# Kernel tuning notes

Hardware: AMD Instinct MI355X
Metric: run time of the kernel (lower is better)

Reference implementation:

```python
import jax, jax.numpy as jnp
import numpy as np

D = 1024
H = 16
DK = D // H
TB = 64  # temporal_bias_dim
SCALE = DK ** -0.5


def setup_inputs() -> dict:
    key = jax.random.key(0)
    ks = jax.random.split(key, 12)
    B, S = 8, 512
    s = 0.02
    return {
        "x": jax.random.normal(ks[0], (B, S, D), jnp.float32),
        "padding_masks": jnp.ones((B, 1, 1, S), jnp.int32),
        "batch_temporal_mat": jax.random.uniform(ks[1], (B, S, S), jnp.float32) * 100.0,
        "wq": jax.random.normal(ks[2], (D, D), jnp.float32) * s,
        "bq": jnp.zeros((D,), jnp.float32),
        "wk": jax.random.normal(ks[3], (D, D), jnp.float32) * s,
        "bk": jnp.zeros((D,), jnp.float32),
        "wv": jax.random.normal(ks[4], (D, D), jnp.float32) * s,
        "bv": jnp.zeros((D,), jnp.float32),
        "w_proj": jax.random.normal(ks[5], (D, D), jnp.float32) * s,
        "b_proj": jnp.zeros((D,), jnp.float32),
        "w_tb1": jax.random.normal(ks[6], (1, TB), jnp.float32) * 0.5,
        "b_tb1": jnp.zeros((TB,), jnp.float32),
        "w_tb2": jax.random.normal(ks[7], (TB, 1), jnp.float32) * 0.5,
        "b_tb2": jnp.zeros((1,), jnp.float32),
    }


def reference(x, padding_masks, batch_temporal_mat, wq, bq, wk, bk, wv, bv,
              w_proj, b_proj, w_tb1, b_tb1, w_tb2, b_tb2):
    B, S, _ = x.shape

    def heads(w, b):
        return (x @ w + b).reshape(B, S, H, DK).transpose(0, 2, 1, 3)  # (B,H,S,DK)

    q, k, v = heads(wq, bq), heads(wk, bk), heads(wv, bv)
    scores = jnp.einsum("bhqd,bhkd->bhqk", q, k) * SCALE  # (B,H,S,S)

    # temporal bias: 1/log(e + t) -> Linear(1,64) -> leaky_relu(0.2) -> Linear(64,1)
    t = 1.0 / jnp.log(jnp.exp(jnp.float32(1.0)) + batch_temporal_mat)  # (B,S,S)
    h = t[..., None] * w_tb1[0] + b_tb1  # (B,S,S,TB)
    h = jnp.where(h >= 0, h, 0.2 * h)
    bias = (h @ w_tb2)[..., 0] + b_tb2[0]  # (B,S,S)
    scores = scores + bias[:, None, :, :]

    neg_inf = jnp.float32(-jnp.inf)
    scores = jnp.where(padding_masks == 0, neg_inf, scores)
    causal = jnp.triu(jnp.ones((S, S), bool), k=1)  # (S,S), add_cls=False
    scores = jnp.where(causal[None, None], neg_inf, scores)

    p_attn = jax.nn.softmax(scores, axis=-1)
    out = jnp.einsum("bhqk,bhkd->bhqd", p_attn, v)
    out = out.transpose(0, 2, 1, 3).reshape(B, S, D)
    out = out @ w_proj + b_proj
    return out
```

## Files before the change

kernel.cpp:

```cpp
#include <hip/hip_runtime.h>
#include <hip/hip_bf16.h>

#define B_  8
#define S_  512
#define D_  1024
#define H_  16
#define DK_ 64
#define TB_ 64
#define SCALE_ 0.125f

typedef __attribute__((ext_vector_type(8))) short          bh8;
typedef __attribute__((ext_vector_type(4))) float          f32x4;
typedef __attribute__((ext_vector_type(8))) unsigned short us8;

__device__ __forceinline__ unsigned short f2bf(float f) {
    unsigned u = __float_as_uint(f);
    unsigned r = 0x7fffu + ((u >> 16) & 1u);
    return (unsigned short)((u + r) >> 16);
}

__device__ __forceinline__ void gl16(const unsigned short* g, unsigned short* l) {
    __builtin_amdgcn_global_load_lds(
        (const __attribute__((address_space(1))) void*)g,
        (__attribute__((address_space(3))) void*)l, 16, 0, 0);
}

__global__ __launch_bounds__(256)
void cvt_x_kernel(const float* __restrict__ in, unsigned short* __restrict__ out, int n8)
{
    int i = blockIdx.x * 256 + threadIdx.x;
    if (i >= n8) return;
    float4 a = *(const float4*)&in[(size_t)i * 8];
    float4 b = *(const float4*)&in[(size_t)i * 8 + 4];
    us8 o;
    o[0] = f2bf(a.x); o[1] = f2bf(a.y); o[2] = f2bf(a.z); o[3] = f2bf(a.w);
    o[4] = f2bf(b.x); o[5] = f2bf(b.y); o[6] = f2bf(b.z); o[7] = f2bf(b.w);
    *(us8*)&out[(size_t)i * 8] = o;
}

__global__ __launch_bounds__(256)
void cvt_wt4_kernel(const float* __restrict__ w0, const float* __restrict__ w1,
                    const float* __restrict__ w2, const float* __restrict__ w3,
                    unsigned short* __restrict__ o0, unsigned short* __restrict__ o1,
                    unsigned short* __restrict__ o2, unsigned short* __restrict__ o3)
{
    __shared__ float t[64][65];
    const int z = blockIdx.z;
    const float* W = (z == 0) ? w0 : (z == 1) ? w1 : (z == 2) ? w2 : w3;
    unsigned short* Wt = (z == 0) ? o0 : (z == 1) ? o1 : (z == 2) ? o2 : o3;
    const int bx = blockIdx.x, by = blockIdx.y;
    const int c  = threadIdx.x & 63;
    const int r0 = threadIdx.x >> 6;
    #pragma unroll
    for (int i = 0; i < 16; ++i) {
        int r = r0 + i * 4;
        t[r][c] = W[(size_t)(by * 64 + r) * 1024 + bx * 64 + c];
    }
    __syncthreads();
    #pragma unroll
    for (int i = 0; i < 16; ++i) {
        int r = r0 + i * 4;
        Wt[(size_t)(bx * 64 + r) * 1024 + by * 64 + c] = f2bf(t[c][r]);
    }
}

__global__ __launch_bounds__(256)
void gemm_qkv_kernel(const unsigned short* __restrict__ A,
                     const unsigned short* __restrict__ Wt,
                     const float* __restrict__ bq, const float* __restrict__ bk,
                     const float* __restrict__ bv,
                     unsigned short* __restrict__ qo,
                     unsigned short* __restrict__ ko,
                     unsigned short* __restrict__ vo)
{
    __shared__ unsigned short As[128 * 64];
    __shared__ unsigned short Bs[128 * 64];
    const int tid  = threadIdx.x;
    const int lane = tid & 63;
    const int wid  = tid >> 6;
    const int wr   = wid >> 1, wc = wid & 1;
    const int row0 = blockIdx.x * 128;
    const int col0 = blockIdx.y * 128;

    f32x4 acc[4][4] = {};

    const int fr = lane & 15;
    const int g  = lane >> 4;
    const int sr = lane >> 3;
    const int sc = ((lane & 7) ^ sr) * 8;

    for (int k0 = 0; k0 < 1024; k0 += 64) {
        #pragma unroll
        for (int i = 0; i < 4; ++i) {
            gl16(&A [(size_t)(row0 + wid * 32 + i * 8 + sr) * 1024 + k0 + sc],
                 &As[(wid * 32 + i * 8) * 64]);
            gl16(&Wt[(size_t)(col0 + wid * 32 + i * 8 + sr) * 1024 + k0 + sc],
                 &Bs[(wid * 32 + i * 8) * 64]);
        }
        __syncthreads();
        #pragma unroll
        for (int ks = 0; ks < 2; ++ks) {
            const int ch = (ks * 4 + g) ^ (fr & 7);
            bh8 af[4], bfr[4];
            #pragma unroll
            for (int r = 0; r < 4; ++r)
                af[r]  = *(const bh8*)&As[(wr * 64 + r * 16 + fr) * 64 + ch * 8];
            #pragma unroll
            for (int c = 0; c < 4; ++c)
                bfr[c] = *(const bh8*)&Bs[(wc * 64 + c * 16 + fr) * 64 + ch * 8];
            #pragma unroll
            for (int r = 0; r < 4; ++r)
                #pragma unroll
                for (int c = 0; c < 4; ++c)
                    acc[r][c] = __builtin_amdgcn_mfma_f32_16x16x32_bf16(
                        af[r], bfr[c], acc[r][c], 0, 0, 0);
        }
        __syncthreads();
    }

    const int nh = col0 >> 10;
    const float* bsel = (nh == 0) ? bq : (nh == 1) ? bk : bv;
    unsigned short* outp = (nh == 0) ? qo : (nh == 1) ? ko : vo;

    #pragma unroll
    for (int r = 0; r < 4; ++r) {
        #pragma unroll
        for (int c = 0; c < 4; ++c) {
            int n  = col0 + wc * 64 + c * 16 + fr;
            int nn = n & 1023;
            float bn = bsel[nn];
            int hh = nn >> 6, dd = nn & 63;
            #pragma unroll
            for (int j = 0; j < 4; ++j) {
                int m = row0 + wr * 64 + r * 16 + g * 4 + j;
                float o = acc[r][c][j] + bn;
                int bb = m >> 9, ss = m & 511;
                if (nh == 2)
                    outp[((size_t)((bb * H_ + hh) * DK_ + dd)) * S_ + ss] = f2bf(o);
                else
                    outp[((size_t)((bb * H_ + hh) * S_ + ss)) * DK_ + dd] = f2bf(o);
            }
        }
    }
}

__global__ __launch_bounds__(256)
void gemm_proj_kernel(const unsigned short* __restrict__ A,
                      const unsigned short* __restrict__ Wt,
                      const float* __restrict__ bias,
                      float* __restrict__ C)
{
    __shared__ unsigned short As[128 * 64];
    __shared__ unsigned short Bs[64 * 64];
    const int tid  = threadIdx.x;
    const int lane = tid & 63;
    const int wid  = tid >> 6;
    const int wr   = wid >> 1, wc = wid & 1;
    const int row0 = blockIdx.x * 128;
    const int col0 = blockIdx.y * 64;

    f32x4 acc[4][2] = {};

    const int fr = lane & 15;
    const int g  = lane >> 4;
    const int sr = lane >> 3;
    const int sc = ((lane & 7) ^ sr) * 8;

    for (int k0 = 0; k0 < 1024; k0 += 64) {
        #pragma unroll
        for (int i = 0; i < 4; ++i)
            gl16(&A [(size_t)(row0 + wid * 32 + i * 8 + sr) * 1024 + k0 + sc],
                 &As[(wid * 32 + i * 8) * 64]);
        #pragma unroll
        for (int i = 0; i < 2; ++i)
            gl16(&Wt[(size_t)(col0 + wid * 16 + i * 8 + sr) * 1024 + k0 + sc],
                 &Bs[(wid * 16 + i * 8) * 64]);
        __syncthreads();
        #pragma unroll
        for (int ks = 0; ks < 2; ++ks) {
            const int ch = (ks * 4 + g) ^ (fr & 7);
            bh8 af[4], bfr[2];
            #pragma unroll
            for (int r = 0; r < 4; ++r)
                af[r]  = *(const bh8*)&As[(wr * 64 + r * 16 + fr) * 64 + ch * 8];
            #pragma unroll
            for (int c = 0; c < 2; ++c)
                bfr[c] = *(const bh8*)&Bs[(wc * 32 + c * 16 + fr) * 64 + ch * 8];
            #pragma unroll
            for (int r = 0; r < 4; ++r)
                #pragma unroll
                for (int c = 0; c < 2; ++c)
                    acc[r][c] = __builtin_amdgcn_mfma_f32_16x16x32_bf16(
                        af[r], bfr[c], acc[r][c], 0, 0, 0);
        }
        __syncthreads();
    }

    #pragma unroll
    for (int r = 0; r < 4; ++r) {
        #pragma unroll
        for (int c = 0; c < 2; ++c) {
            int n = col0 + wc * 32 + c * 16 + fr;
            float bn = bias[n];
            #pragma unroll
            for (int j = 0; j < 4; ++j) {
                int m = row0 + wr * 64 + r * 16 + g * 4 + j;
                C[(size_t)m * 1024 + n] = acc[r][c][j] + bn;
            }
        }
    }
}

__global__ __launch_bounds__(256)
void tbias_kernel(const float* __restrict__ tm, const int* __restrict__ pmask,
                  const float* __restrict__ w1, const float* __restrict__ b1,
                  const float* __restrict__ w2, const float* __restrict__ b2,
                  float* __restrict__ bias)
{
    __shared__ float sw1[TB_], sb1[TB_], sw2[TB_];
    if (threadIdx.x < TB_) {
        sw1[threadIdx.x] = w1[threadIdx.x];
        sb1[threadIdx.x] = b1[threadIdx.x];
        sw2[threadIdx.x] = w2[threadIdx.x];
    }
    __syncthreads();
    const float ec  = 2.7182818284590452f;
    const float b2v = b2[0];
    const int n = B_ * S_ * S_;
    for (int i = blockIdx.x * blockDim.x + threadIdx.x; i < n;
         i += gridDim.x * blockDim.x) {
        int bb = i >> 18;
        int jj = i & (S_ - 1);
        float t   = 1.0f / logf(ec + tm[i]);
        float acc = b2v;
        #pragma unroll
        for (int j = 0; j < TB_; ++j) {
            float h = fmaf(t, sw1[j], sb1[j]);
            h = (h >= 0.f) ? h : 0.2f * h;
            acc = fmaf(h, sw2[j], acc);
        }
        bias[i] = (pmask[bb * S_ + jj] == 0) ? -1e30f : acc;
    }
}

__global__ __launch_bounds__(256)
void attn_kernel(const unsigned short* __restrict__ q,
                 const unsigned short* __restrict__ k,
                 const unsigned short* __restrict__ vt,
                 const float* __restrict__ biasm,
                 unsigned short* __restrict__ outb)
{
    __shared__ unsigned short Kl[64][72];
    __shared__ unsigned short Vl[64][72];
    __shared__ unsigned short Pl[64][72];

    const int tid  = threadIdx.x;
    const int lane = tid & 63;
    const int w    = tid >> 6;
    const int lin = (blockIdx.x & 7) * 128 + (blockIdx.x >> 3);
    const int h   = lin & 15;
    const int qt  = (lin >> 4) & 7;
    const int b   = lin >> 7;
    const int q0  = qt * 64;

    const int l15 = lane & 15;
    const int g   = lane >> 4;

    const size_t hb  = (size_t)(b * H_ + h) * S_;
    const unsigned short* kbase  = k  + hb * DK_;
    const unsigned short* vtbase = vt + ((size_t)(b * H_ + h) * DK_) * S_;

    const int qrow_a = q0 + w * 16 + l15;
    bh8 aq0 = *(const bh8*)&q[(hb + qrow_a) * DK_ +      g * 8];
    bh8 aq1 = *(const bh8*)&q[(hb + qrow_a) * DK_ + 32 + g * 8];

    const int qd = q0 + w * 16 + g * 4;

    f32x4 acc_o[4] = {};
    float m_run[4] = { -1e30f, -1e30f, -1e30f, -1e30f };
    float l_run[4] = {};

    for (int kt = 0; kt <= qt; ++kt) {
        __syncthreads();
        #pragma unroll
        for (int s = 0; s < 2; ++s) {
            int u  = tid + s * 256;
            int r  = u >> 3;
            int c8 = (u & 7) * 8;
            *(int4*)&Kl[r][c8] = *(const int4*)&kbase [(size_t)(kt * 64 + r) * DK_ + c8];
            *(int4*)&Vl[r][c8] = *(const int4*)&vtbase[(size_t)r * S_ + kt * 64 + c8];
        }
        __syncthreads();

        f32x4 sc[4];
        #pragma unroll
        for (int c = 0; c < 4; ++c) {
            bh8 bk0 = *(const bh8*)&Kl[c * 16 + l15][     g * 8];
            bh8 bk1 = *(const bh8*)&Kl[c * 16 + l15][32 + g * 8];
            f32x4 z = {};
            z = __builtin_amdgcn_mfma_f32_16x16x32_bf16(aq0, bk0, z, 0, 0, 0);
            sc[c] = __builtin_amdgcn_mfma_f32_16x16x32_bf16(aq1, bk1, z, 0, 0, 0);
        }

        float sv[4][4];
        #pragma unroll
        for (int j = 0; j < 4; ++j) {
            const float* br = biasm + ((size_t)b * S_ + qd + j) * S_ + kt * 64;
            #pragma unroll
            for (int c = 0; c < 4; ++c)
                sv[c][j] = fmaf(sc[c][j], SCALE_, br[c * 16 + l15]);
        }
        if (kt == qt) {
            #pragma unroll
            for (int c = 0; c < 4; ++c) {
                int kloc = c * 16 + l15;
                #pragma unroll
                for (int j = 0; j < 4; ++j)
                    if (kloc > w * 16 + g * 4 + j) sv[c][j] = -1e30f;
            }
        }

        #pragma unroll
        for (int j = 0; j < 4; ++j) {
            float mt = fmaxf(fmaxf(sv[0][j], sv[1][j]), fmaxf(sv[2][j], sv[3][j]));
            mt = fmaxf(mt, __shfl_xor(mt, 1));
            mt = fmaxf(mt, __shfl_xor(mt, 2));
            mt = fmaxf(mt, __shfl_xor(mt, 4));
            mt = fmaxf(mt, __shfl_xor(mt, 8));
            float m_new = fmaxf(m_run[j], mt);
            float resc  = __expf(m_run[j] - m_new);
            float psum  = 0.f;
            #pragma unroll
            for (int c = 0; c < 4; ++c) {
                float p = __expf(sv[c][j] - m_new);
                Pl[w * 16 + g * 4 + j][c * 16 + l15] = f2bf(p);
                psum += p;
            }
            psum += __shfl_xor(psum, 1);
            psum += __shfl_xor(psum, 2);
            psum += __shfl_xor(psum, 4);
            psum += __shfl_xor(psum, 8);
            l_run[j] = l_run[j] * resc + psum;
            m_run[j] = m_new;
            acc_o[0][j] *= resc; acc_o[1][j] *= resc;
            acc_o[2][j] *= resc; acc_o[3][j] *= resc;
        }

        asm volatile("s_waitcnt lgkmcnt(0)" ::: "memory");

        bh8 ap0 = *(const bh8*)&Pl[w * 16 + l15][     g * 8];
        bh8 ap1 = *(const bh8*)&Pl[w * 16 + l15][32 + g * 8];
        #pragma unroll
        for (int c2 = 0; c2 < 4; ++c2) {
            bh8 bv0 = *(const bh8*)&Vl[c2 * 16 + l15][     g * 8];
            bh8 bv1 = *(const bh8*)&Vl[c2 * 16 + l15][32 + g * 8];
            acc_o[c2] = __builtin_amdgcn_mfma_f32_16x16x32_bf16(ap0, bv0, acc_o[c2], 0, 0, 0);
            acc_o[c2] = __builtin_amdgcn_mfma_f32_16x16x32_bf16(ap1, bv1, acc_o[c2], 0, 0, 0);
        }
    }

    #pragma unroll
    for (int j = 0; j < 4; ++j) {
        float linv = 1.f / l_run[j];
        #pragma unroll
        for (int c2 = 0; c2 < 4; ++c2)
            outb[((size_t)(b * S_ + qd + j)) * D_ + h * DK_ + c2 * 16 + l15] =
                f2bf(acc_o[c2][j] * linv);
    }
}

extern "C" void kernel_launch(void* const* d_in, const int* in_sizes, int n_in,
                              void* d_out, int out_size, void* d_ws, size_t ws_size,
                              hipStream_t stream)
{
    const float* x     = (const float*)d_in[0];
    const int*   pm    = (const int*)  d_in[1];
    const float* tm    = (const float*)d_in[2];
    const float* wq    = (const float*)d_in[3];
    const float* bq    = (const float*)d_in[4];
    const float* wk    = (const float*)d_in[5];
    const float* bk    = (const float*)d_in[6];
    const float* wv    = (const float*)d_in[7];
    const float* bv    = (const float*)d_in[8];
    const float* wp    = (const float*)d_in[9];
    const float* bp    = (const float*)d_in[10];
    const float* w_tb1 = (const float*)d_in[11];
    const float* b_tb1 = (const float*)d_in[12];
    const float* w_tb2 = (const float*)d_in[13];
    const float* b_tb2 = (const float*)d_in[14];

    char* wsb = (char*)d_ws;
    const size_t MB = 1u << 20;
    unsigned short* xb   = (unsigned short*)wsb;
    unsigned short* wqkv = (unsigned short*)(wsb + 8  * MB);
    unsigned short* wtp  = (unsigned short*)(wsb + 14 * MB);
    unsigned short* qw   = (unsigned short*)(wsb + 16 * MB);
    unsigned short* kw   = (unsigned short*)(wsb + 24 * MB);
    unsigned short* vtw  = (unsigned short*)(wsb + 32 * MB);
    float*          bw   = (float*)        (wsb + 40 * MB);

    cvt_x_kernel<<<2048, 256, 0, stream>>>(x, xb, 524288);
    dim3 gw(16, 16, 4);
    cvt_wt4_kernel<<<gw, 256, 0, stream>>>(wq, wk, wv, wp,
                                           wqkv, wqkv + 1048576, wqkv + 2097152, wtp);

    dim3 gqkv(32, 24);
    gemm_qkv_kernel<<<gqkv, 256, 0, stream>>>(xb, wqkv, bq, bk, bv, qw, kw, vtw);

    tbias_kernel<<<2048, 256, 0, stream>>>(tm, pm, w_tb1, b_tb1, w_tb2, b_tb2, bw);

    attn_kernel<<<1024, 256, 0, stream>>>(qw, kw, vtw, bw, xb );

    dim3 gp(32, 16);
    gemm_proj_kernel<<<gp, 256, 0, stream>>>(xb, wtp, bp, (float*)d_out);
}
```

Measured before the change: 225.3 us.

## Double-buffer LDS in QKV and projection GEMMs with smaller 64x64 tiles

Both GEMM kernels now use 64x64 output tiles with two LDS buffers. The next K-slice is loaded asynchronously into LDS while the current one is computed, so only one barrier is needed per iteration. Smaller tiles quadruple the QKV grid and double the projection grid, which adds parallelism across CUs. In exchange, operand reuse per block drops and global and L2 traffic rise, since each wave now issues 4 MFMAs per k-step instead of 16 or 8.

```diff
diff --git a/kernel.cpp b/kernel.cpp
--- a/kernel.cpp
+++ b/kernel.cpp
@@ -64,6 +64,33 @@
     }
 }
 
+#define GEMM_STAGE(buf, k0) do {                                         \
+    gl16(Arow + (k0),            &As[buf][(w * 16    ) * 64]);           \
+    gl16(Arow + (k0) + 8 * 1024, &As[buf][(w * 16 + 8) * 64]);           \
+    gl16(Brow + (k0),            &Bs[buf][(w * 16    ) * 64]);           \
+    gl16(Brow + (k0) + 8 * 1024, &Bs[buf][(w * 16 + 8) * 64]);           \
+} while (0)
+
+#define GEMM_COMPUTE(buf) do {                                           \
+    _Pragma("unroll")                                                    \
+    for (int ks = 0; ks < 2; ++ks) {                                     \
+        const int ch = (ks * 4 + g) ^ (fr & 7);                          \
+        bh8 af[2], bf[2];                                                \
+        _Pragma("unroll")                                                \
+        for (int r = 0; r < 2; ++r)                                      \
+            af[r] = *(const bh8*)&As[buf][(wr * 32 + r * 16 + fr) * 64 + ch * 8]; \
+        _Pragma("unroll")                                                \
+        for (int c = 0; c < 2; ++c)                                      \
+            bf[c] = *(const bh8*)&Bs[buf][(wc * 32 + c * 16 + fr) * 64 + ch * 8]; \
+        _Pragma("unroll")                                                \
+        for (int r = 0; r < 2; ++r)                                      \
+            _Pragma("unroll")                                            \
+            for (int c = 0; c < 2; ++c)                                  \
+                acc[r][c] = __builtin_amdgcn_mfma_f32_16x16x32_bf16(     \
+                    af[r], bf[c], acc[r][c], 0, 0, 0);                   \
+    }                                                                    \
+} while (0)
+
 __global__ __launch_bounds__(256)
 void gemm_qkv_kernel(const unsigned short* __restrict__ A,
                      const unsigned short* __restrict__ Wt,
@@ -73,66 +100,51 @@
                      unsigned short* __restrict__ ko,
                      unsigned short* __restrict__ vo)
 {
-    __shared__ unsigned short As[128 * 64];
-    __shared__ unsigned short Bs[128 * 64];
+    __shared__ unsigned short As[2][64 * 64];
+    __shared__ unsigned short Bs[2][64 * 64];
     const int tid  = threadIdx.x;
     const int lane = tid & 63;
-    const int wid  = tid >> 6;
-    const int wr   = wid >> 1, wc = wid & 1;
-    const int row0 = blockIdx.x * 128;
-    const int col0 = blockIdx.y * 128;
-
-    f32x4 acc[4][4] = {};
-
+    const int w    = tid >> 6;
+    const int wr   = w >> 1, wc = w & 1;
+    const int row0 = blockIdx.x * 64;
+    const int col0 = blockIdx.y * 64;
+
+    f32x4 acc[2][2] = {};
     const int fr = lane & 15;
     const int g  = lane >> 4;
     const int sr = lane >> 3;
     const int sc = ((lane & 7) ^ sr) * 8;
 
-    for (int k0 = 0; k0 < 1024; k0 += 64) {
-        #pragma unroll
-        for (int i = 0; i < 4; ++i) {
-            gl16(&A [(size_t)(row0 + wid * 32 + i * 8 + sr) * 1024 + k0 + sc],
-                 &As[(wid * 32 + i * 8) * 64]);
-            gl16(&Wt[(size_t)(col0 + wid * 32 + i * 8 + sr) * 1024 + k0 + sc],
-                 &Bs[(wid * 32 + i * 8) * 64]);
-        }
+    const unsigned short* Arow = A  + (size_t)(row0 + w * 16 + sr) * 1024 + sc;
+    const unsigned short* Brow = Wt + (size_t)(col0 + w * 16 + sr) * 1024 + sc;
+
+    GEMM_STAGE(0, 0);
+    __syncthreads();
+    int cur = 0;
+    #pragma unroll 1
+    for (int t = 0; t < 15; ++t) {
+        GEMM_STAGE(cur ^ 1, (t + 1) * 64);
+        GEMM_COMPUTE(cur);
         __syncthreads();
-        #pragma unroll
-        for (int ks = 0; ks < 2; ++ks) {
-            const int ch = (ks * 4 + g) ^ (fr & 7);
-            bh8 af[4], bfr[4];
-            #pragma unroll
-            for (int r = 0; r < 4; ++r)
-                af[r]  = *(const bh8*)&As[(wr * 64 + r * 16 + fr) * 64 + ch * 8];
-            #pragma unroll
-            for (int c = 0; c < 4; ++c)
-                bfr[c] = *(const bh8*)&Bs[(wc * 64 + c * 16 + fr) * 64 + ch * 8];
-            #pragma unroll
-            for (int r = 0; r < 4; ++r)
-                #pragma unroll
-                for (int c = 0; c < 4; ++c)
-                    acc[r][c] = __builtin_amdgcn_mfma_f32_16x16x32_bf16(
-                        af[r], bfr[c], acc[r][c], 0, 0, 0);
-        }
-        __syncthreads();
-    }
+        cur ^= 1;
+    }
+    GEMM_COMPUTE(cur);
 
     const int nh = col0 >> 10;
     const float* bsel = (nh == 0) ? bq : (nh == 1) ? bk : bv;
     unsigned short* outp = (nh == 0) ? qo : (nh == 1) ? ko : vo;
 
     #pragma unroll
-    for (int r = 0; r < 4; ++r) {
-        #pragma unroll
-        for (int c = 0; c < 4; ++c) {
-            int n  = col0 + wc * 64 + c * 16 + fr;
+    for (int r = 0; r < 2; ++r) {
+        #pragma unroll
+        for (int c = 0; c < 2; ++c) {
+            int n  = col0 + wc * 32 + c * 16 + fr;
             int nn = n & 1023;
             float bn = bsel[nn];
             int hh = nn >> 6, dd = nn & 63;
             #pragma unroll
             for (int j = 0; j < 4; ++j) {
-                int m = row0 + wr * 64 + r * 16 + g * 4 + j;
+                int m = row0 + wr * 32 + r * 16 + g * 4 + j;
                 float o = acc[r][c][j] + bn;
                 int bb = m >> 9, ss = m & 511;
                 if (nh == 2)
@@ -150,61 +162,45 @@
                       const float* __restrict__ bias,
                       float* __restrict__ C)
 {
-    __shared__ unsigned short As[128 * 64];
-    __shared__ unsigned short Bs[64 * 64];
+    __shared__ unsigned short As[2][64 * 64];
+    __shared__ unsigned short Bs[2][64 * 64];
     const int tid  = threadIdx.x;
     const int lane = tid & 63;
-    const int wid  = tid >> 6;
-    const int wr   = wid >> 1, wc = wid & 1;
-    const int row0 = blockIdx.x * 128;
+    const int w    = tid >> 6;
+    const int wr   = w >> 1, wc = w & 1;
+    const int row0 = blockIdx.x * 64;
     const int col0 = blockIdx.y * 64;
 
-    f32x4 acc[4][2] = {};
-
+    f32x4 acc[2][2] = {};
     const int fr = lane & 15;
     const int g  = lane >> 4;
     const int sr = lane >> 3;
     const int sc = ((lane & 7) ^ sr) * 8;
 
-    for (int k0 = 0; k0 < 1024; k0 += 64) {
-        #pragma unroll
-        for (int i = 0; i < 4; ++i)
-            gl16(&A [(size_t)(row0 + wid * 32 + i * 8 + sr) * 1024 + k0 + sc],
-                 &As[(wid * 32 + i * 8) * 64]);
-        #pragma unroll
-        for (int i = 0; i < 2; ++i)
-            gl16(&Wt[(size_t)(col0 + wid * 16 + i * 8 + sr) * 1024 + k0 + sc],
-                 &Bs[(wid * 16 + i * 8) * 64]);
+    const unsigned short* Arow = A  + (size_t)(row0 + w * 16 + sr) * 1024 + sc;
+    const unsigned short* Brow = Wt + (size_t)(col0 + w * 16 + sr) * 1024 + sc;
+
+    GEMM_STAGE(0, 0);
+    __syncthreads();
+    int cur = 0;
+    #pragma unroll 1
+    for (int t = 0; t < 15; ++t) {
+        GEMM_STAGE(cur ^ 1, (t + 1) * 64);
+        GEMM_COMPUTE(cur);
         __syncthreads();
-        #pragma unroll
-        for (int ks = 0; ks < 2; ++ks) {
-            const int ch = (ks * 4 + g) ^ (fr & 7);
-            bh8 af[4], bfr[2];
-            #pragma unroll
-            for (int r = 0; r < 4; ++r)
-                af[r]  = *(const bh8*)&As[(wr * 64 + r * 16 + fr) * 64 + ch * 8];
-            #pragma unroll
-            for (int c = 0; c < 2; ++c)
-                bfr[c] = *(const bh8*)&Bs[(wc * 32 + c * 16 + fr) * 64 + ch * 8];
-            #pragma unroll
-            for (int r = 0; r < 4; ++r)
-                #pragma unroll
-                for (int c = 0; c < 2; ++c)
-                    acc[r][c] = __builtin_amdgcn_mfma_f32_16x16x32_bf16(
-                        af[r], bfr[c], acc[r][c], 0, 0, 0);
-        }
-        __syncthreads();
-    }
+        cur ^= 1;
+    }
+    GEMM_COMPUTE(cur);
 
     #pragma unroll
-    for (int r = 0; r < 4; ++r) {
+    for (int r = 0; r < 2; ++r) {
         #pragma unroll
         for (int c = 0; c < 2; ++c) {
             int n = col0 + wc * 32 + c * 16 + fr;
             float bn = bias[n];
             #pragma unroll
             for (int j = 0; j < 4; ++j) {
-                int m = row0 + wr * 64 + r * 16 + g * 4 + j;
+                int m = row0 + wr * 32 + r * 16 + g * 4 + j;
                 C[(size_t)m * 1024 + n] = acc[r][c][j] + bn;
             }
         }
@@ -404,13 +400,13 @@
     cvt_wt4_kernel<<<gw, 256, 0, stream>>>(wq, wk, wv, wp,
                                            wqkv, wqkv + 1048576, wqkv + 2097152, wtp);
 
-    dim3 gqkv(32, 24);
+    dim3 gqkv(64, 48);
     gemm_qkv_kernel<<<gqkv, 256, 0, stream>>>(xb, wqkv, bq, bk, bv, qw, kw, vtw);
 
     tbias_kernel<<<2048, 256, 0, stream>>>(tm, pm, w_tb1, b_tb1, w_tb2, b_tb2, bw);
 
     attn_kernel<<<1024, 256, 0, stream>>>(qw, kw, vtw, bw, xb );
 
-    dim3 gp(32, 16);
+    dim3 gp(64, 16);
     gemm_proj_kernel<<<gp, 256, 0, stream>>>(xb, wtp, bp, (float*)d_out);
 }
```

After: 219.1 us. -2.8%, faster.
